# Performance work log

Hardware: AMD Instinct MI355X
Metric: run time of the kernel (lower is better)

The kernel has to match this reference:

```python
import jax, jax.numpy as jnp
import numpy as np

SEQ, DIN, DOUT, RANK = 8192, 4096, 4096, 16

def setup_inputs() -> dict:
    key = jax.random.key(0)
    ks = jax.random.split(key, 5)
    return {
        "x": jax.random.normal(ks[0], (SEQ, DIN), dtype=jnp.float32),
        "W": jax.random.normal(ks[1], (DIN, DOUT), dtype=jnp.float32) * (1.0 / np.sqrt(DIN)),
        "bias": jax.random.normal(ks[2], (DOUT,), dtype=jnp.float32),
        "A_buffer": jax.random.normal(ks[3], (DIN, RANK), dtype=jnp.float32) * (1.0 / np.sqrt(DIN)),
        "B_buffer": jax.random.normal(ks[4], (RANK, DOUT), dtype=jnp.float32),
    }

def reference(x, W, bias, A_buffer, B_buffer):
    # base linear GEMM: [seq, in] @ [in, out] -> [seq, out]
    base_output = jnp.dot(x, W)
    # LoRA path: two low-rank GEMMs fused-added onto base output
    lora_a = jnp.dot(x, A_buffer)            # [seq, rank]
    output = base_output + jnp.dot(lora_a, B_buffer)  # [seq, out]
    # module returns (output, output_bias) with bias passed through separately
    return (output, bias)
```

## Files before the change

### kernel.cpp

```cpp
#include <hip/hip_runtime.h>
#include <cstdint>
#include <cstddef>


#define SEQ  8192
#define DIN  4096
#define DOUT 4096
#define RANK 16

typedef __attribute__((ext_vector_type(8))) __bf16 bf16x8;
typedef __attribute__((ext_vector_type(4))) float f32x4;
typedef __attribute__((ext_vector_type(8))) unsigned short ushort8;

#define CAST_BLOCKS ((SEQ * DIN) / (256 * 8))
#define WEFF_BLOCKS ((DOUT / 64) * (DIN / 64))

__device__ __forceinline__ unsigned short f32_to_bf16_rne(float f) {
  union { float f; unsigned int u; } cv;
  cv.f = f;
  unsigned int u = cv.u;
  u += 0x7FFFu + ((u >> 16) & 1u);
  return (unsigned short)(u >> 16);
}

__global__ __launch_bounds__(256) void prep_kernel(
    const float* __restrict__ x, unsigned short* __restrict__ xb,
    const float* __restrict__ bias, float* __restrict__ bias_out,
    const float* __restrict__ W, const float* __restrict__ A,
    const float* __restrict__ B, unsigned short* __restrict__ WT) {
  __shared__ float sBf[RANK][64];
  __shared__ float sAf[64][RANK];
  __shared__ unsigned short sT[64][65];
  const int bid = blockIdx.x;
  const int t = threadIdx.x;

  if (bid < CAST_BLOCKS) {
    const int tid = bid * 256 + t;
    const float4* x4 = (const float4*)x;
    float4 v0 = x4[(size_t)tid * 2 + 0];
    float4 v1 = x4[(size_t)tid * 2 + 1];
    ushort8 o;
    o[0] = f32_to_bf16_rne(v0.x); o[1] = f32_to_bf16_rne(v0.y);
    o[2] = f32_to_bf16_rne(v0.z); o[3] = f32_to_bf16_rne(v0.w);
    o[4] = f32_to_bf16_rne(v1.x); o[5] = f32_to_bf16_rne(v1.y);
    o[6] = f32_to_bf16_rne(v1.z); o[7] = f32_to_bf16_rne(v1.w);
    *(ushort8*)(xb + (size_t)tid * 8) = o;
    if (tid < DOUT) bias_out[tid] = bias[tid];
    return;
  }

  const int b  = bid - CAST_BLOCKS;
  const int n0 = (b & 63) * 64;
  const int k0 = (b >> 6) * 64;

  for (int idx = t; idx < RANK * 64; idx += 256) {
    int r = idx >> 6, c = idx & 63;
    sBf[r][c] = B[(size_t)r * DOUT + n0 + c];
  }
  for (int idx = t; idx < 64 * RANK; idx += 256) {
    int i = idx >> 4, r = idx & 15;
    sAf[i][r] = A[(size_t)(k0 + i) * RANK + r];
  }
  __syncthreads();

  const int c   = t & 63;
  const int sub = t >> 6;
  #pragma unroll
  for (int p = 0; p < 16; ++p) {
    const int ki = p * 4 + sub;
    float acc = W[(size_t)(k0 + ki) * DOUT + n0 + c];
    #pragma unroll
    for (int r = 0; r < RANK; ++r) acc += sAf[ki][r] * sBf[r][c];
    sT[ki][c] = f32_to_bf16_rne(acc);
  }
  __syncthreads();
  #pragma unroll
  for (int p = 0; p < 16; ++p) {
    const int ni = p * 4 + sub;
    WT[(size_t)(n0 + ni) * DIN + k0 + c] = sT[c][ni];
  }
}

#define BM 128
#define BN 128
#define BK 64

__global__ __launch_bounds__(256) void gemm_bt_kernel(
    const unsigned short* __restrict__ xb, const unsigned short* __restrict__ wt,
    float* __restrict__ out) {
  __shared__ unsigned short sA[BM * BK];
  __shared__ unsigned short sB[BN * BK];
  const int t = threadIdx.x;
  const int n0 = blockIdx.x * BN;
  const int m0 = blockIdx.y * BM;

  const int lane = t & 63;
  const int w    = t >> 6;
  const int wr   = w >> 1;
  const int wc   = w & 1;
  const int quad = lane >> 4;
  const int lcol = lane & 15;

  const int g     = (lane & 7) ^ ((lane >> 3) & 7);
  const int rbase = w * 8 + (lane >> 3);
  const unsigned short* gA[4];
  const unsigned short* gB[4];
  #pragma unroll
  for (int j = 0; j < 4; ++j) {
    gA[j] = xb + (size_t)(m0 + rbase + j * 32) * DIN + g * 8;
    gB[j] = wt + (size_t)(n0 + rbase + j * 32) * DIN + g * 8;
  }
  unsigned short* lA[4];
  unsigned short* lB[4];
  #pragma unroll
  for (int j = 0; j < 4; ++j) {
    lA[j] = (unsigned short*)sA + (j * 256 + t) * 8;
    lB[j] = (unsigned short*)sB + (j * 256 + t) * 8;
  }

  f32x4 acc[4][4] = {};

  const int xorv = lcol & 7;
  const int arow = (wr * 64 + lcol) * BK;
  const int brow = (wc * 64 + lcol) * BK;

  for (int kt = 0; kt < DIN; kt += BK) {
    #pragma unroll
    for (int j = 0; j < 4; ++j)
      __builtin_amdgcn_global_load_lds(
          (const __attribute__((address_space(1))) void*)(gA[j] + kt),
          (__attribute__((address_space(3))) void*)lA[j], 16, 0, 0);
    #pragma unroll
    for (int j = 0; j < 4; ++j)
      __builtin_amdgcn_global_load_lds(
          (const __attribute__((address_space(1))) void*)(gB[j] + kt),
          (__attribute__((address_space(3))) void*)lB[j], 16, 0, 0);
    __syncthreads();

    #pragma unroll
    for (int kk = 0; kk < 2; ++kk) {
      const int cpos = ((quad + 4 * kk) ^ xorv) * 8;
      bf16x8 a[4], b[4];
      #pragma unroll
      for (int i = 0; i < 4; ++i)
        a[i] = *(const bf16x8*)((const unsigned short*)sA + arow + i * 16 * BK + cpos);
      #pragma unroll
      for (int j = 0; j < 4; ++j)
        b[j] = *(const bf16x8*)((const unsigned short*)sB + brow + j * 16 * BK + cpos);
      #pragma unroll
      for (int i = 0; i < 4; ++i)
        #pragma unroll
        for (int j = 0; j < 4; ++j)
          acc[i][j] = __builtin_amdgcn_mfma_f32_16x16x32_bf16(a[i], b[j], acc[i][j], 0, 0, 0);
    }
    __syncthreads();
  }

  const int row_base = m0 + wr * 64 + quad * 4;
  const int col_base = n0 + wc * 64 + lcol;
  #pragma unroll
  for (int i = 0; i < 4; ++i)
    #pragma unroll
    for (int j = 0; j < 4; ++j)
      #pragma unroll
      for (int r = 0; r < 4; ++r)
        out[(size_t)(row_base + i * 16 + r) * DOUT + (col_base + j * 16)] =
            acc[i][j][r];
}

extern "C" void kernel_launch(void* const* d_in, const int* in_sizes, int n_in,
                              void* d_out, int out_size, void* d_ws, size_t ws_size,
                              hipStream_t stream) {
  const float* x    = (const float*)d_in[0];
  const float* W    = (const float*)d_in[1];
  const float* bias = (const float*)d_in[2];
  const float* A    = (const float*)d_in[3];
  const float* B    = (const float*)d_in[4];
  float* out      = (float*)d_out;
  float* bias_out = out + (size_t)SEQ * DOUT;

  unsigned short* xb = (unsigned short*)d_ws;
  unsigned short* wt = xb + (size_t)SEQ * DIN;

  prep_kernel<<<CAST_BLOCKS + WEFF_BLOCKS, 256, 0, stream>>>(
      x, xb, bias, bias_out, W, A, B, wt);
  gemm_bt_kernel<<<dim3(DOUT / BN, SEQ / BM), 256, 0, stream>>>(xb, wt, out);
}
```

Baseline: 574.9 us.

## Rewrite GEMM with 256x256 tiles, double-buffered LDS pipeline, and split prep kernels

The GEMM moves from 128x128 tiles with 4 waves to 256x256 tiles with 8 waves. It adds a double-buffered LDS prefetch schedule with manual s_waitcnt and barriers, MFMA priority boosts, and a blockIdx swizzle for L2 locality. The prep work is split into separate cast and weight-fold kernels. The weight-fold kernel now keeps B in registers, reads A as float4 from LDS, and writes the transposed weights with 16-byte vector stores. The goal is better MFMA utilisation and less memory and latency stall, at the cost of fragile hand-tuned wait counts and higher register and LDS pressure.

```diff
diff --git a/kernel.cpp b/kernel.cpp
--- a/kernel.cpp
+++ b/kernel.cpp
@@ -23,149 +23,226 @@
   return (unsigned short)(u >> 16);
 }
 
-__global__ __launch_bounds__(256) void prep_kernel(
+__global__ __launch_bounds__(256) void cast_kernel(
     const float* __restrict__ x, unsigned short* __restrict__ xb,
-    const float* __restrict__ bias, float* __restrict__ bias_out,
+    const float* __restrict__ bias, float* __restrict__ bias_out) {
+  const int tid = blockIdx.x * 256 + threadIdx.x;
+  const float4* x4 = (const float4*)x;
+  float4 v0 = x4[(size_t)tid * 2 + 0];
+  float4 v1 = x4[(size_t)tid * 2 + 1];
+  ushort8 o;
+  o[0] = f32_to_bf16_rne(v0.x); o[1] = f32_to_bf16_rne(v0.y);
+  o[2] = f32_to_bf16_rne(v0.z); o[3] = f32_to_bf16_rne(v0.w);
+  o[4] = f32_to_bf16_rne(v1.x); o[5] = f32_to_bf16_rne(v1.y);
+  o[6] = f32_to_bf16_rne(v1.z); o[7] = f32_to_bf16_rne(v1.w);
+  *(ushort8*)(xb + (size_t)tid * 8) = o;
+  if (tid < DOUT) bias_out[tid] = bias[tid];
+}
+
+__global__ __launch_bounds__(256) void weff_kernel(
     const float* __restrict__ W, const float* __restrict__ A,
     const float* __restrict__ B, unsigned short* __restrict__ WT) {
   __shared__ float sBf[RANK][64];
-  __shared__ float sAf[64][RANK];
+  __shared__ float sAf[64][16];
   __shared__ unsigned short sT[64][65];
-  const int bid = blockIdx.x;
+  const int blk = blockIdx.x;
+  const int n0 = (blk & 63) * 64;
+  const int k0 = (blk >> 6) * 64;
   const int t = threadIdx.x;
 
-  if (bid < CAST_BLOCKS) {
-    const int tid = bid * 256 + t;
-    const float4* x4 = (const float4*)x;
-    float4 v0 = x4[(size_t)tid * 2 + 0];
-    float4 v1 = x4[(size_t)tid * 2 + 1];
-    ushort8 o;
-    o[0] = f32_to_bf16_rne(v0.x); o[1] = f32_to_bf16_rne(v0.y);
-    o[2] = f32_to_bf16_rne(v0.z); o[3] = f32_to_bf16_rne(v0.w);
-    o[4] = f32_to_bf16_rne(v1.x); o[5] = f32_to_bf16_rne(v1.y);
-    o[6] = f32_to_bf16_rne(v1.z); o[7] = f32_to_bf16_rne(v1.w);
-    *(ushort8*)(xb + (size_t)tid * 8) = o;
-    if (tid < DOUT) bias_out[tid] = bias[tid];
-    return;
-  }
-
-  const int b  = bid - CAST_BLOCKS;
-  const int n0 = (b & 63) * 64;
-  const int k0 = (b >> 6) * 64;
-
-  for (int idx = t; idx < RANK * 64; idx += 256) {
-    int r = idx >> 6, c = idx & 63;
-    sBf[r][c] = B[(size_t)r * DOUT + n0 + c];
-  }
-  for (int idx = t; idx < 64 * RANK; idx += 256) {
-    int i = idx >> 4, r = idx & 15;
-    sAf[i][r] = A[(size_t)(k0 + i) * RANK + r];
+  #pragma unroll
+  for (int pass = 0; pass < 4; ++pass) {
+    const int idx = pass * 256 + t;
+    sBf[idx >> 6][idx & 63] = B[(size_t)(idx >> 6) * DOUT + n0 + (idx & 63)];
+    sAf[idx >> 4][idx & 15] = A[(size_t)(k0 + (idx >> 4)) * RANK + (idx & 15)];
   }
   __syncthreads();
 
   const int c   = t & 63;
   const int sub = t >> 6;
+  float breg[16];
+  #pragma unroll
+  for (int r = 0; r < 16; ++r) breg[r] = sBf[r][c];
+
   #pragma unroll
   for (int p = 0; p < 16; ++p) {
     const int ki = p * 4 + sub;
+    const float4* ar = (const float4*)sAf[ki];
+    const float4 a0 = ar[0], a1 = ar[1], a2 = ar[2], a3 = ar[3];
     float acc = W[(size_t)(k0 + ki) * DOUT + n0 + c];
+    acc += a0.x * breg[0]  + a0.y * breg[1]  + a0.z * breg[2]  + a0.w * breg[3];
+    acc += a1.x * breg[4]  + a1.y * breg[5]  + a1.z * breg[6]  + a1.w * breg[7];
+    acc += a2.x * breg[8]  + a2.y * breg[9]  + a2.z * breg[10] + a2.w * breg[11];
+    acc += a3.x * breg[12] + a3.y * breg[13] + a3.z * breg[14] + a3.w * breg[15];
+    sT[ki][c] = f32_to_bf16_rne(acc);
+  }
+  __syncthreads();
+
+  #pragma unroll
+  for (int s = 0; s < 2; ++s) {
+    const int ni = (t >> 3) + s * 32;
+    const int cc = t & 7;
+    ushort8 o;
     #pragma unroll
-    for (int r = 0; r < RANK; ++r) acc += sAf[ki][r] * sBf[r][c];
-    sT[ki][c] = f32_to_bf16_rne(acc);
-  }
-  __syncthreads();
-  #pragma unroll
-  for (int p = 0; p < 16; ++p) {
-    const int ni = p * 4 + sub;
-    WT[(size_t)(n0 + ni) * DIN + k0 + c] = sT[c][ni];
-  }
-}
-
-#define BM 128
-#define BN 128
+    for (int u = 0; u < 8; ++u) o[u] = sT[cc * 8 + u][ni];
+    *(ushort8*)(WT + (size_t)(n0 + ni) * DIN + k0 + cc * 8) = o;
+  }
+}
+
+#define BM 256
+#define BN 256
 #define BK 64
-
-__global__ __launch_bounds__(256) void gemm_bt_kernel(
+#define GRID_X (DOUT / BN)
+#define GRID_Y (SEQ / BM)
+#define NWG (GRID_X * GRID_Y)
+
+#define BARX()   asm volatile("s_barrier" ::: "memory")
+#define LGKM(n)  asm volatile("s_waitcnt lgkmcnt(" #n ")" ::: "memory")
+#define VMW(n)   asm volatile("s_waitcnt vmcnt(" #n ")" ::: "memory")
+
+#define STAGE_AH(BUF, H, KOFF)                                                 \
+  __builtin_amdgcn_global_load_lds(                                            \
+      (const __attribute__((address_space(1))) void*)(gA + (size_t)((H)*128 + 0)  * DIN + (KOFF)),  \
+      (__attribute__((address_space(3))) void*)(sA + (BUF)*16384 + (H)*8192 + 0    + t*8), 16, 0, 0);\
+  __builtin_amdgcn_global_load_lds(                                            \
+      (const __attribute__((address_space(1))) void*)(gA + (size_t)((H)*128 + 64) * DIN + (KOFF)),  \
+      (__attribute__((address_space(3))) void*)(sA + (BUF)*16384 + (H)*8192 + 4096 + t*8), 16, 0, 0);
+
+#define STAGE_BH(BUF, H, KOFF)                                                 \
+  __builtin_amdgcn_global_load_lds(                                            \
+      (const __attribute__((address_space(1))) void*)(gB + (size_t)((H)*128 + 0)  * DIN + (KOFF)),  \
+      (__attribute__((address_space(3))) void*)(sB + (BUF)*16384 + (H)*8192 + 0    + t*8), 16, 0, 0);\
+  __builtin_amdgcn_global_load_lds(                                            \
+      (const __attribute__((address_space(1))) void*)(gB + (size_t)((H)*128 + 64) * DIN + (KOFF)),  \
+      (__attribute__((address_space(3))) void*)(sB + (BUF)*16384 + (H)*8192 + 4096 + t*8), 16, 0, 0);
+
+#define MFMA(A, B, C) __builtin_amdgcn_mfma_f32_16x16x32_bf16(A, B, C, 0, 0, 0)
+
+#define KTILE(CUR, KOFF1, KOFF2, S1, S234, W1, W2, W4)                         \
+  {                                                                            \
+    const int ab_ = (CUR) * 16384;                                             \
+    const int bb_ = (CUR) * 16384;                                             \
+    bf16x8 a[4][2], b01[2][2], b23[2][2];                                      \
+                                     \
+    _Pragma("unroll") for (int i = 0; i < 4; ++i) {                            \
+      a[i][0] = *(const bf16x8*)(sA + ab_ + aoff[i] + cp0);                    \
+      a[i][1] = *(const bf16x8*)(sA + ab_ + aoff[i] + cp1); }                  \
+    _Pragma("unroll") for (int j = 0; j < 2; ++j) {                            \
+      b01[j][0] = *(const bf16x8*)(sB + bb_ + boff[j] + cp0);                  \
+      b01[j][1] = *(const bf16x8*)(sB + bb_ + boff[j] + cp1); }                \
+    if (S1) { STAGE_AH((CUR) ^ 1, 1, KOFF1); }                                 \
+    LGKM(8);                                                                   \
+    BARX(); LGKM(0);                                                           \
+    __builtin_amdgcn_s_setprio(1);                                             \
+    _Pragma("unroll") for (int i = 0; i < 4; ++i)                              \
+      _Pragma("unroll") for (int j = 0; j < 2; ++j) {                          \
+        acc[i][j] = MFMA(a[i][0], b01[j][0], acc[i][j]);                       \
+        acc[i][j] = MFMA(a[i][1], b01[j][1], acc[i][j]); }                     \
+    __builtin_amdgcn_s_setprio(0);                                             \
+    VMW(W1); BARX();                                                           \
+                                      \
+    _Pragma("unroll") for (int j = 0; j < 2; ++j) {                            \
+      b23[j][0] = *(const bf16x8*)(sB + bb_ + boff[j + 2] + cp0);              \
+      b23[j][1] = *(const bf16x8*)(sB + bb_ + boff[j + 2] + cp1); }            \
+    if (S234) { STAGE_BH((CUR), 0, KOFF2); }                                   \
+    BARX(); LGKM(0);                                                           \
+    __builtin_amdgcn_s_setprio(1);                                             \
+    _Pragma("unroll") for (int i = 0; i < 4; ++i)                              \
+      _Pragma("unroll") for (int j = 0; j < 2; ++j) {                          \
+        acc[i][j + 2] = MFMA(a[i][0], b23[j][0], acc[i][j + 2]);               \
+        acc[i][j + 2] = MFMA(a[i][1], b23[j][1], acc[i][j + 2]); }             \
+    __builtin_amdgcn_s_setprio(0);                                             \
+    VMW(W2); BARX();                                                           \
+                                      \
+    _Pragma("unroll") for (int i = 0; i < 4; ++i) {                            \
+      a[i][0] = *(const bf16x8*)(sA + ab_ + aoff[i + 4] + cp0);                \
+      a[i][1] = *(const bf16x8*)(sA + ab_ + aoff[i + 4] + cp1); }              \
+    if (S234) { STAGE_AH((CUR), 0, KOFF2); }                                   \
+    BARX(); LGKM(0);                                                           \
+    __builtin_amdgcn_s_setprio(1);                                             \
+    _Pragma("unroll") for (int i = 0; i < 4; ++i)                              \
+      _Pragma("unroll") for (int j = 0; j < 2; ++j) {                          \
+        acc[i + 4][j + 2] = MFMA(a[i][0], b23[j][0], acc[i + 4][j + 2]);       \
+        acc[i + 4][j + 2] = MFMA(a[i][1], b23[j][1], acc[i + 4][j + 2]); }     \
+    __builtin_amdgcn_s_setprio(0);                                             \
+    BARX();                                                                    \
+           \
+    if (S234) { STAGE_BH((CUR), 1, KOFF2); }                                   \
+    __builtin_amdgcn_s_setprio(1);                                             \
+    _Pragma("unroll") for (int i = 0; i < 4; ++i)                              \
+      _Pragma("unroll") for (int j = 0; j < 2; ++j) {                          \
+        acc[i + 4][j] = MFMA(a[i][0], b01[j][0], acc[i + 4][j]);               \
+        acc[i + 4][j] = MFMA(a[i][1], b01[j][1], acc[i + 4][j]); }             \
+    __builtin_amdgcn_s_setprio(0);                                             \
+    VMW(W4); BARX();                                                           \
+  }
+
+__global__ __launch_bounds__(512, 2) void gemm_bt_kernel(
     const unsigned short* __restrict__ xb, const unsigned short* __restrict__ wt,
     float* __restrict__ out) {
-  __shared__ unsigned short sA[BM * BK];
-  __shared__ unsigned short sB[BN * BK];
+  __shared__ unsigned short sA[2 * BM * BK];
+  __shared__ unsigned short sB[2 * BN * BK];
+
   const int t = threadIdx.x;
-  const int n0 = blockIdx.x * BN;
-  const int m0 = blockIdx.y * BM;
-
   const int lane = t & 63;
   const int w    = t >> 6;
-  const int wr   = w >> 1;
-  const int wc   = w & 1;
+  const int wr   = w >> 2;
+  const int wc   = w & 3;
   const int quad = lane >> 4;
   const int lcol = lane & 15;
 
-  const int g     = (lane & 7) ^ ((lane >> 3) & 7);
-  const int rbase = w * 8 + (lane >> 3);
-  const unsigned short* gA[4];
-  const unsigned short* gB[4];
-  #pragma unroll
-  for (int j = 0; j < 4; ++j) {
-    gA[j] = xb + (size_t)(m0 + rbase + j * 32) * DIN + g * 8;
-    gB[j] = wt + (size_t)(n0 + rbase + j * 32) * DIN + g * 8;
-  }
-  unsigned short* lA[4];
-  unsigned short* lB[4];
-  #pragma unroll
-  for (int j = 0; j < 4; ++j) {
-    lA[j] = (unsigned short*)sA + (j * 256 + t) * 8;
-    lB[j] = (unsigned short*)sB + (j * 256 + t) * 8;
-  }
-
-  f32x4 acc[4][4] = {};
+  const int lid = blockIdx.y * GRID_X + blockIdx.x;
+  const int swz = (lid & 7) * (NWG / 8) + (lid >> 3);
+  const int n0 = (swz & (GRID_X - 1)) * BN;
+  const int m0 = (swz / GRID_X) * BM;
+
+  const int g    = (lane & 7) ^ (lane >> 3);
+  const int srow = w * 8 + (lane >> 3);
+  const unsigned short* gA = xb + (size_t)(m0 + srow) * DIN + g * 8;
+  const unsigned short* gB = wt + (size_t)(n0 + srow) * DIN + g * 8;
 
   const int xorv = lcol & 7;
-  const int arow = (wr * 64 + lcol) * BK;
-  const int brow = (wc * 64 + lcol) * BK;
-
-  for (int kt = 0; kt < DIN; kt += BK) {
+  const int cp0  = (quad ^ xorv) * 8;
+  const int cp1  = cp0 ^ 32;
+  int aoff[8], boff[4];
+  #pragma unroll
+  for (int i = 0; i < 8; ++i)
+    aoff[i] = ((i >> 2) * 128 + wr * 64 + (i & 3) * 16 + lcol) * 64;
+  #pragma unroll
+  for (int j = 0; j < 4; ++j)
+    boff[j] = ((j >> 1) * 128 + wc * 32 + (j & 1) * 16 + lcol) * 64;
+
+  f32x4 acc[8][4] = {};
+
+  STAGE_AH(0, 0, 0);  STAGE_BH(0, 0, 0);  STAGE_BH(0, 1, 0);  STAGE_AH(0, 1, 0);
+  STAGE_AH(1, 0, 64); STAGE_BH(1, 0, 64); STAGE_BH(1, 1, 64); STAGE_AH(1, 1, 64);
+  VMW(12);
+  BARX();
+
+  KTILE(0, 64, 128, 0, 1, 10, 10, 10);
+
+  #pragma unroll 2
+  for (int tt = 1; tt < 62; ++tt) {
+    const int cur = tt & 1;
+    const int koff1 = (tt + 1) * BK;
+    const int koff2 = (tt + 2) * BK;
+    KTILE(cur, koff1, koff2, 1, 1, 10, 10, 10);
+  }
+
+  KTILE(0, 63 * BK, 0, 1, 0, 10, 8, 6);
+  KTILE(1, 0, 0, 0, 0, 2, 0, 0);
+
+  #pragma unroll
+  for (int i = 0; i < 8; ++i) {
+    const int rb = m0 + (i >> 2) * 128 + wr * 64 + (i & 3) * 16 + quad * 4;
     #pragma unroll
-    for (int j = 0; j < 4; ++j)
-      __builtin_amdgcn_global_load_lds(
-          (const __attribute__((address_space(1))) void*)(gA[j] + kt),
-          (__attribute__((address_space(3))) void*)lA[j], 16, 0, 0);
-    #pragma unroll
-    for (int j = 0; j < 4; ++j)
-      __builtin_amdgcn_global_load_lds(
-          (const __attribute__((address_space(1))) void*)(gB[j] + kt),
-          (__attribute__((address_space(3))) void*)lB[j], 16, 0, 0);
-    __syncthreads();
-
-    #pragma unroll
-    for (int kk = 0; kk < 2; ++kk) {
-      const int cpos = ((quad + 4 * kk) ^ xorv) * 8;
-      bf16x8 a[4], b[4];
-      #pragma unroll
-      for (int i = 0; i < 4; ++i)
-        a[i] = *(const bf16x8*)((const unsigned short*)sA + arow + i * 16 * BK + cpos);
-      #pragma unroll
-      for (int j = 0; j < 4; ++j)
-        b[j] = *(const bf16x8*)((const unsigned short*)sB + brow + j * 16 * BK + cpos);
-      #pragma unroll
-      for (int i = 0; i < 4; ++i)
-        #pragma unroll
-        for (int j = 0; j < 4; ++j)
-          acc[i][j] = __builtin_amdgcn_mfma_f32_16x16x32_bf16(a[i], b[j], acc[i][j], 0, 0, 0);
-    }
-    __syncthreads();
-  }
-
-  const int row_base = m0 + wr * 64 + quad * 4;
-  const int col_base = n0 + wc * 64 + lcol;
-  #pragma unroll
-  for (int i = 0; i < 4; ++i)
-    #pragma unroll
-    for (int j = 0; j < 4; ++j)
+    for (int j = 0; j < 4; ++j) {
+      const int cb = n0 + (j >> 1) * 128 + wc * 32 + (j & 1) * 16 + lcol;
       #pragma unroll
       for (int r = 0; r < 4; ++r)
-        out[(size_t)(row_base + i * 16 + r) * DOUT + (col_base + j * 16)] =
-            acc[i][j][r];
+        out[(size_t)(rb + r) * DOUT + cb] = acc[i][j][r];
+    }
+  }
 }
 
 extern "C" void kernel_launch(void* const* d_in, const int* in_sizes, int n_in,
@@ -182,7 +259,7 @@
   unsigned short* xb = (unsigned short*)d_ws;
   unsigned short* wt = xb + (size_t)SEQ * DIN;
 
-  prep_kernel<<<CAST_BLOCKS + WEFF_BLOCKS, 256, 0, stream>>>(
-      x, xb, bias, bias_out, W, A, B, wt);
-  gemm_bt_kernel<<<dim3(DOUT / BN, SEQ / BM), 256, 0, stream>>>(xb, wt, out);
-}
+  cast_kernel<<<CAST_BLOCKS, 256, 0, stream>>>(x, xb, bias, bias_out);
+  weff_kernel<<<WEFF_BLOCKS, 256, 0, stream>>>(W, A, B, wt);
+  gemm_bt_kernel<<<dim3(GRID_X, GRID_Y), 512, 0, stream>>>(xb, wt, out);
+}
```

Result: faster. 518.3 us (-9.8%).
